# Kernel tuning notes

Hardware: AMD Instinct MI355X
Metric: run time of the kernel (lower is better)

The kernel has to match this reference:

```python
import jax, jax.numpy as jnp
import numpy as np

VOCAB = 1000000
EMBED_DIM = 64


def setup_inputs() -> dict:
    key = jax.random.key(0)
    embeddings = jax.random.normal(key, (VOCAB, EMBED_DIM), dtype=jnp.float32)
    return {"embeddings": embeddings, "user_id": 12345, "top_n": 10}


def reference(embeddings, user_id, top_n):
    # target_embedding = embedding_layer(user_id): [d]
    target = embeddings[user_id]  # [d]
    # cosine_similarity(target[None, :], all_embeddings): [V]
    dot = embeddings @ target  # [V]
    norm_t = jnp.linalg.norm(target)  # scalar (norm over axis=-1 of [1, d])
    norm_all = jnp.linalg.norm(embeddings, axis=-1)  # [V]
    sims = dot / (norm_t * norm_all)
    # tf.nn.top_k with k = top_n + 1, then drop the first (self) match
    top_vals, top_idx = jax.lax.top_k(sims, top_n + 1)
    return top_vals[1:], top_idx[1:]
```

## Files before the change

kernel.cpp:

```cpp
#include <hip/hip_runtime.h>
#include <cmath>
#include <climits>

#define EMBED 64
#define KTOP 11
#define NB   512
#define BLOCK1 256
#define NW1  (BLOCK1 / 64)
#define BLOCK2 256
#define NW2  (BLOCK2 / 64)

__device__ __forceinline__ void topk_insert(float (&vals)[KTOP], int (&idxs)[KTOP],
                                            float v, int i) {
  float last = vals[KTOP - 1];
  if (v < last) return;
  if (v == last && i >= idxs[KTOP - 1]) return;
  float cv = v; int ci = i;
#pragma unroll
  for (int j = 0; j < KTOP; ++j) {
    bool better = (cv > vals[j]) || (cv == vals[j] && ci < idxs[j]);
    if (better) {
      float tv = vals[j]; int ti = idxs[j];
      vals[j] = cv; idxs[j] = ci;
      cv = tv; ci = ti;
    }
  }
}

__device__ __forceinline__ void wave_merge(float (&vals)[KTOP], int (&idxs)[KTOP],
                                           float* wv, int* wi, int lane) {
#pragma unroll
  for (int round = 0; round < KTOP; ++round) {
    float v = vals[0]; int i = idxs[0]; int l = lane;
#pragma unroll
    for (int off = 32; off > 0; off >>= 1) {
      float ov = __shfl_xor(v, off, 64);
      int   oi = __shfl_xor(i, off, 64);
      int   ol = __shfl_xor(l, off, 64);
      if (ov > v || (ov == v && oi < i)) { v = ov; i = oi; l = ol; }
    }
    if (l == lane) {
#pragma unroll
      for (int j = 0; j < KTOP - 1; ++j) { vals[j] = vals[j + 1]; idxs[j] = idxs[j + 1]; }
      vals[KTOP - 1] = -INFINITY; idxs[KTOP - 1] = INT_MAX;
    }
    if (lane == 0) { wv[round] = v; wi[round] = i; }
  }
}

__global__ __launch_bounds__(BLOCK1, 2) void sim_pass1(
    const float* __restrict__ emb, const int* __restrict__ user_id,
    float* __restrict__ cand_val, int* __restrict__ cand_idx, int V) {
  __shared__ float wv[NW1 * KTOP];
  __shared__ int   wi[NW1 * KTOP];

  const int lane = threadIdx.x & 63;
  const int wid  = threadIdx.x >> 6;
  const int uid  = *user_id;

  const float4 tgt = ((const float4*)(emb + (size_t)uid * EMBED))[lane & 15];

  float vals[KTOP]; int idxs[KTOP];
#pragma unroll
  for (int j = 0; j < KTOP; ++j) { vals[j] = -INFINITY; idxs[j] = INT_MAX; }

  const int gw = blockIdx.x * NW1 + wid;
  const int nW = NB * NW1;
  const int nTiles = (V + 63) >> 6;
  const float4* base = (const float4*)emb;
  const size_t maxQ = (size_t)V * 16 - 1;

  for (int tile = gw; tile < nTiles; tile += nW) {
    const size_t q0 = (size_t)tile * 1024 + lane;
    float4 v[16];
#pragma unroll
    for (int j = 0; j < 16; ++j) {
      size_t q = q0 + (size_t)j * 64;
      if (q > maxQ) q = maxQ;
      v[j] = base[q];
    }

    float d[16], n[16];
#pragma unroll
    for (int j = 0; j < 16; ++j) {
      float4 x = v[j];
      float dd =        x.x * tgt.x;
      dd = fmaf(x.y, tgt.y, dd); dd = fmaf(x.z, tgt.z, dd); dd = fmaf(x.w, tgt.w, dd);
      float nn =        x.x * x.x;
      nn = fmaf(x.y, x.y, nn);   nn = fmaf(x.z, x.z, nn);   nn = fmaf(x.w, x.w, nn);
      d[j] = dd; n[j] = nn;
    }

#pragma unroll
    for (int st = 0; st < 4; ++st) {
      const int m = 1 << st;
      const int b = (lane >> st) & 1;
#pragma unroll
      for (int k = 0; k < (16 >> (st + 1)); ++k) {
        float dk = b ? d[2 * k + 1] : d[2 * k];
        float ds = b ? d[2 * k]     : d[2 * k + 1];
        float nk = b ? n[2 * k + 1] : n[2 * k];
        float ns = b ? n[2 * k]     : n[2 * k + 1];
        d[k] = dk + __shfl_xor(ds, m, 64);
        n[k] = nk + __shfl_xor(ns, m, 64);
      }
    }

    const int r = (tile << 6) + ((lane & 15) << 2) + (lane >> 4);
    if (r < V)
      topk_insert(vals, idxs, d[0] / sqrtf(n[0]), r);
  }

  wave_merge(vals, idxs, &wv[wid * KTOP], &wi[wid * KTOP], lane);
  __syncthreads();

  if (wid == 0) {
    float v = (lane < NW1 * KTOP) ? wv[lane] : -INFINITY;
    int   i = (lane < NW1 * KTOP) ? wi[lane] : INT_MAX;
#pragma unroll
    for (int round = 0; round < KTOP; ++round) {
      float bv = v; int bi = i; int bl = lane;
#pragma unroll
      for (int off = 32; off > 0; off >>= 1) {
        float ov = __shfl_xor(bv, off, 64);
        int   oi = __shfl_xor(bi, off, 64);
        int   ol = __shfl_xor(bl, off, 64);
        if (ov > bv || (ov == bv && oi < bi)) { bv = ov; bi = oi; bl = ol; }
      }
      if (bl == lane) { v = -INFINITY; i = INT_MAX; }
      if (lane == 0) {
        cand_val[blockIdx.x * KTOP + round] = bv;
        cand_idx[blockIdx.x * KTOP + round] = bi;
      }
    }
  }
}

__global__ __launch_bounds__(BLOCK2) void sim_pass2(
    const float* __restrict__ emb, const int* __restrict__ user_id,
    const float* __restrict__ cand_val, const int* __restrict__ cand_idx,
    float* __restrict__ out, int topn, int ncand) {
  __shared__ float wv[NW2 * KTOP];
  __shared__ int   wi[NW2 * KTOP];
  __shared__ float s_nt;

  const int lane = threadIdx.x & 63;
  const int wid  = threadIdx.x >> 6;

  if (wid == 0) {
    const int uid = *user_id;
    float x = (lane < EMBED) ? emb[(size_t)uid * EMBED + lane] : 0.f;
    float s = x * x;
#pragma unroll
    for (int off = 32; off > 0; off >>= 1) s += __shfl_xor(s, off, 64);
    if (lane == 0) s_nt = sqrtf(s);
  }

  float vals[KTOP]; int idxs[KTOP];
#pragma unroll
  for (int j = 0; j < KTOP; ++j) { vals[j] = -INFINITY; idxs[j] = INT_MAX; }

  for (int c = threadIdx.x; c < ncand; c += BLOCK2)
    topk_insert(vals, idxs, cand_val[c], cand_idx[c]);

  wave_merge(vals, idxs, &wv[wid * KTOP], &wi[wid * KTOP], lane);
  __syncthreads();

  if (wid == 0) {
    float v = (lane < NW2 * KTOP) ? wv[lane] : -INFINITY;
    int   i = (lane < NW2 * KTOP) ? wi[lane] : INT_MAX;
    const float nt = s_nt;
#pragma unroll
    for (int round = 0; round < KTOP; ++round) {
      float bv = v; int bi = i; int bl = lane;
#pragma unroll
      for (int off = 32; off > 0; off >>= 1) {
        float ov = __shfl_xor(bv, off, 64);
        int   oi = __shfl_xor(bi, off, 64);
        int   ol = __shfl_xor(bl, off, 64);
        if (ov > bv || (ov == bv && oi < bi)) { bv = ov; bi = oi; bl = ol; }
      }
      if (bl == lane) { v = -INFINITY; i = INT_MAX; }
      if (lane == 0 && round >= 1 && round <= topn) {
        out[round - 1]        = bv / nt;
        out[topn + round - 1] = (float)bi;
      }
    }
  }
}

extern "C" void kernel_launch(void* const* d_in, const int* in_sizes, int n_in,
                              void* d_out, int out_size, void* d_ws, size_t ws_size,
                              hipStream_t stream) {
  const float* emb = (const float*)d_in[0];
  const int*   uid = (const int*)d_in[1];
  const int V    = in_sizes[0] / EMBED;
  const int topn = out_size / 2;

  float* cand_val = (float*)d_ws;
  int*   cand_idx = (int*)((char*)d_ws + (size_t)NB * KTOP * sizeof(float));

  sim_pass1<<<NB, BLOCK1, 0, stream>>>(emb, uid, cand_val, cand_idx, V);
  sim_pass2<<<1, BLOCK2, 0, stream>>>(emb, uid, cand_val, cand_idx,
                                      (float*)d_out, topn, NB * KTOP);
}
```

Baseline: 405.7 us.

## Split each tile between async LDS DMA and direct register loads with double buffering

Each wave's 64-row tile is split in half. The first 32 rows are prefetched one iteration ahead into a per-wave double-buffered LDS region using global_load_lds. The other 32 rows are loaded straight into registers, with manual s_waitcnt counts ordering the two streams. The aim is to keep more memory traffic in flight and hide load latency on a bandwidth-bound scan. The cost is 64KB of LDS per block, which may limit occupancy, and fragile hand-written waitcnt and parity logic that decides which lanes insert into the top-k.

```diff
diff --git a/kernel.cpp b/kernel.cpp
--- a/kernel.cpp
+++ b/kernel.cpp
@@ -9,6 +9,11 @@
 #define NW1  (BLOCK1 / 64)
 #define BLOCK2 256
 #define NW2  (BLOCK2 / 64)
+#define ATILE 8192
+#define SUPER 16384
+
+typedef const __attribute__((address_space(1))) void gv_t;
+typedef __attribute__((address_space(3))) void lv_t;
 
 __device__ __forceinline__ void topk_insert(float (&vals)[KTOP], int (&idxs)[KTOP],
                                             float v, int i) {
@@ -48,17 +53,39 @@
   }
 }
 
+__device__ __forceinline__ void dmaA(const char* g, size_t byteBase,
+                                     int lane, char* lds, size_t maxOff) {
+  if (byteBase + ATILE - 16 <= maxOff) {
+#pragma unroll
+    for (int j = 0; j < 8; ++j)
+      __builtin_amdgcn_global_load_lds(
+          (gv_t*)(g + byteBase + (size_t)j * 1024 + (size_t)lane * 16),
+          (lv_t*)(lds + j * 1024), 16, 0, 0);
+  } else {
+#pragma unroll
+    for (int j = 0; j < 8; ++j) {
+      size_t off = byteBase + (size_t)j * 1024 + (size_t)lane * 16;
+      if (off > maxOff) off = maxOff;
+      __builtin_amdgcn_global_load_lds(
+          (gv_t*)(g + off), (lv_t*)(lds + j * 1024), 16, 0, 0);
+    }
+  }
+}
+
 __global__ __launch_bounds__(BLOCK1, 2) void sim_pass1(
     const float* __restrict__ emb, const int* __restrict__ user_id,
     float* __restrict__ cand_val, int* __restrict__ cand_idx, int V) {
-  __shared__ float wv[NW1 * KTOP];
-  __shared__ int   wi[NW1 * KTOP];
+  __shared__ __align__(16) char smem[2 * NW1 * ATILE];
 
   const int lane = threadIdx.x & 63;
   const int wid  = threadIdx.x >> 6;
   const int uid  = *user_id;
 
-  const float4 tgt = ((const float4*)(emb + (size_t)uid * EMBED))[lane & 15];
+  const float4* trow = (const float4*)(emb + (size_t)uid * EMBED);
+  float4 tvA[8];
+#pragma unroll
+  for (int j = 0; j < 8; ++j) tvA[j] = trow[(lane >> 5) * 8 + ((j + lane) & 7)];
+  const float4 tgtB = trow[lane & 15];
 
   float vals[KTOP]; int idxs[KTOP];
 #pragma unroll
@@ -66,51 +93,97 @@
 
   const int gw = blockIdx.x * NW1 + wid;
   const int nW = NB * NW1;
-  const int nTiles = (V + 63) >> 6;
+  const int nSuper = (V + 63) >> 6;
+  const char* g = (const char*)emb;
   const float4* base = (const float4*)emb;
-  const size_t maxQ = (size_t)V * 16 - 1;
-
-  for (int tile = gw; tile < nTiles; tile += nW) {
-    const size_t q0 = (size_t)tile * 1024 + lane;
-    float4 v[16];
-#pragma unroll
-    for (int j = 0; j < 16; ++j) {
+  const size_t maxOff = (size_t)V * 256 - 16;
+  const size_t maxQ   = (size_t)V * 16 - 1;
+  char* myLds = smem + wid * (2 * ATILE);
+
+  int p = 0;
+  int s = gw;
+  if (s < nSuper) dmaA(g, (size_t)s * SUPER, lane, myLds, maxOff);
+
+  int par = 0;
+  for (; s < nSuper; s += nW, par ^= 1) {
+    const size_t q0 = (size_t)s * 1024 + 512 + lane;
+    float4 v[8];
+#pragma unroll
+    for (int j = 0; j < 8; ++j) {
       size_t q = q0 + (size_t)j * 64;
       if (q > maxQ) q = maxQ;
       v[j] = base[q];
     }
-
-    float d[16], n[16];
-#pragma unroll
-    for (int j = 0; j < 16; ++j) {
-      float4 x = v[j];
-      float dd =        x.x * tgt.x;
-      dd = fmaf(x.y, tgt.y, dd); dd = fmaf(x.z, tgt.z, dd); dd = fmaf(x.w, tgt.w, dd);
-      float nn =        x.x * x.x;
-      nn = fmaf(x.y, x.y, nn);   nn = fmaf(x.z, x.z, nn);   nn = fmaf(x.w, x.w, nn);
-      d[j] = dd; n[j] = nn;
-    }
-
-#pragma unroll
-    for (int st = 0; st < 4; ++st) {
-      const int m = 1 << st;
-      const int b = (lane >> st) & 1;
-#pragma unroll
-      for (int k = 0; k < (16 >> (st + 1)); ++k) {
-        float dk = b ? d[2 * k + 1] : d[2 * k];
-        float ds = b ? d[2 * k]     : d[2 * k + 1];
-        float nk = b ? n[2 * k + 1] : n[2 * k];
-        float ns = b ? n[2 * k]     : n[2 * k + 1];
-        d[k] = dk + __shfl_xor(ds, m, 64);
-        n[k] = nk + __shfl_xor(ns, m, 64);
-      }
-    }
-
-    const int r = (tile << 6) + ((lane & 15) << 2) + (lane >> 4);
-    if (r < V)
-      topk_insert(vals, idxs, d[0] / sqrtf(n[0]), r);
-  }
-
+    asm volatile("" ::: "memory");
+
+    const int next = s + nW;
+    const bool pf = next < nSuper;
+    if (pf) {
+      dmaA(g, (size_t)next * SUPER, lane, myLds + (p ^ 1) * ATILE, maxOff);
+      asm volatile("s_waitcnt vmcnt(16)" ::: "memory");
+    } else {
+      asm volatile("s_waitcnt vmcnt(8)" ::: "memory");
+    }
+
+    {
+      const char* lb = myLds + p * ATILE + (lane & 31) * 256 + (lane >> 5) * 128;
+      float dot = 0.f, nr = 0.f;
+#pragma unroll
+      for (int j = 0; j < 8; ++j) {
+        float4 x = *(const float4*)(lb + ((j + lane) & 7) * 16);
+        float4 t = tvA[j];
+        dot = fmaf(x.x, t.x, dot); dot = fmaf(x.y, t.y, dot);
+        dot = fmaf(x.z, t.z, dot); dot = fmaf(x.w, t.w, dot);
+        nr  = fmaf(x.x, x.x, nr);  nr  = fmaf(x.y, x.y, nr);
+        nr  = fmaf(x.z, x.z, nr);  nr  = fmaf(x.w, x.w, nr);
+      }
+      dot += __shfl_xor(dot, 32, 64);
+      nr  += __shfl_xor(nr,  32, 64);
+      const int r = (s << 6) + (lane & 31);
+      if ((lane >> 5) == par && r < V)
+        topk_insert(vals, idxs, dot / sqrtf(nr), r);
+    }
+
+    if (pf) asm volatile("s_waitcnt vmcnt(8)" ::: "memory");
+    else    asm volatile("s_waitcnt vmcnt(0)" ::: "memory");
+
+    {
+      float d[8], n[8];
+#pragma unroll
+      for (int j = 0; j < 8; ++j) {
+        float4 x = v[j];
+        float dd =        x.x * tgtB.x;
+        dd = fmaf(x.y, tgtB.y, dd); dd = fmaf(x.z, tgtB.z, dd); dd = fmaf(x.w, tgtB.w, dd);
+        float nn =        x.x * x.x;
+        nn = fmaf(x.y, x.y, nn);    nn = fmaf(x.z, x.z, nn);    nn = fmaf(x.w, x.w, nn);
+        d[j] = dd; n[j] = nn;
+      }
+#pragma unroll
+      for (int st = 0; st < 3; ++st) {
+        const int m = 1 << st;
+        const int b = (lane >> st) & 1;
+#pragma unroll
+        for (int k = 0; k < (8 >> (st + 1)); ++k) {
+          float dk = b ? d[2 * k + 1] : d[2 * k];
+          float ds = b ? d[2 * k]     : d[2 * k + 1];
+          float nk = b ? n[2 * k + 1] : n[2 * k];
+          float ns = b ? n[2 * k]     : n[2 * k + 1];
+          d[k] = dk + __shfl_xor(ds, m, 64);
+          n[k] = nk + __shfl_xor(ns, m, 64);
+        }
+      }
+      d[0] += __shfl_xor(d[0], 8, 64);
+      n[0] += __shfl_xor(n[0], 8, 64);
+      const int r = (s << 6) + 32 + ((lane & 7) << 2) + (lane >> 4);
+      if (((lane >> 3) & 1) == par && r < V)
+        topk_insert(vals, idxs, d[0] / sqrtf(n[0]), r);
+    }
+    p ^= 1;
+  }
+
+  __syncthreads();
+  float* wv = (float*)smem;
+  int*   wi = (int*)(smem + NW1 * KTOP * sizeof(float));
   wave_merge(vals, idxs, &wv[wid * KTOP], &wi[wid * KTOP], lane);
   __syncthreads();
 
```

Measured after the change: 410.0 us. Within noise of the previous version (+1.0%).
